# Kernel optimization log

Measured on AMD Instinct MI355X. Metric: run time of the kernel, lower is better.

## Reference

```python
import jax, jax.numpy as jnp
import numpy as np

B, S, W = 128, 128, 16          # batch, sentence len, chars per word
WV, CV = 50000, 500             # word / char vocab sizes
WE, CE, H = 128, 64, 256        # word emb, char emb (=char lstm hidden), sentence lstm hidden
NT = 25                         # tagset size
K = NT + 2                      # +START/+STOP for CRF
F = 4                           # feature_size = len(features)-1 ('CEM' consumed)
START, STOP = NT, NT + 1


def setup_inputs() -> dict:
    key = jax.random.key(0)
    ks = jax.random.split(key, 32)
    p = lambda i, shape: jax.random.normal(ks[i], shape, jnp.float32) * 0.1
    inp = {}
    inp["words2ix"] = jax.random.randint(ks[0], (B, S), 0, WV)
    inp["chars2ix"] = jax.random.randint(ks[1], (B, S, W), 0, CV)
    inp["features"] = jax.random.uniform(ks[2], (B, F, S), jnp.float32)
    lens = jax.random.randint(ks[3], (B,), S // 2, S + 1)
    inp["attention_mask"] = (jnp.arange(S)[None, :] < lens[:, None]).astype(jnp.int32)
    inp["word_emb"] = p(4, (WV, WE))
    inp["char_emb"] = p(5, (CV, CE))
    for d, i0 in (("f", 6), ("b", 10)):
        inp[f"char_Wih_{d}"] = p(i0, (4 * CE, CE))
        inp[f"char_Whh_{d}"] = p(i0 + 1, (4 * CE, CE))
        inp[f"char_bih_{d}"] = p(i0 + 2, (4 * CE,))
        inp[f"char_bhh_{d}"] = p(i0 + 3, (4 * CE,))
    inp["char_out_W"] = p(14, (CE, 2 * CE))
    inp["char_out_b"] = p(15, (CE,))
    inp["feat_W"] = p(16, (H // 2, F))
    inp["feat_b"] = p(17, (H // 2,))
    IN = WE + CE + H // 2  # 320
    for d, i0 in (("f", 18), ("b", 22)):
        inp[f"lstm_Wih_{d}"] = p(i0, (4 * H, IN))
        inp[f"lstm_Whh_{d}"] = p(i0 + 1, (4 * H, H))
        inp[f"lstm_bih_{d}"] = p(i0 + 2, (4 * H,))
        inp[f"lstm_bhh_{d}"] = p(i0 + 3, (4 * H,))
    FC = 2 * H + CE + H // 2  # 704
    inp["tag_W"] = p(26, (K, FC))
    inp["tag_b"] = p(27, (K,))
    inp["trans"] = p(28, (K, K))  # trans[i, j] = score of transition i -> j
    return inp


def _lstm(x, Wih, Whh, bih, bhh, reverse=False):
    # x: [T, N, In] -> (outputs [T, N, H], final hidden [N, H]); PyTorch gate order i,f,g,o
    Hd = Whh.shape[1]
    N = x.shape[1]

    def step(carry, xt):
        h, c = carry
        g = xt @ Wih.T + bih + h @ Whh.T + bhh
        i, f, gg, o = jnp.split(g, 4, axis=-1)
        c = jax.nn.sigmoid(f) * c + jax.nn.sigmoid(i) * jnp.tanh(gg)
        h = jax.nn.sigmoid(o) * jnp.tanh(c)
        return (h, c), h

    init = (jnp.zeros((N, Hd), x.dtype), jnp.zeros((N, Hd), x.dtype))
    (hT, _), hs = jax.lax.scan(step, init, x, reverse=reverse)
    return hs, hT


def _viterbi(feats, mask, trans):
    # feats: [B, S, K] emissions; mask: [B, S] prefix mask; trans: [K, K]
    score0 = feats[:, 0] + trans[START][None, :]  # [B, K]

    def step(score, inputs):
        feat_t, m_t = inputs                               # [B,K], [B]
        cand = score[:, :, None] + trans[None, :, :]       # [B, K_prev, K_cur]
        best = jnp.max(cand, axis=1) + feat_t              # [B, K]
        bp = jnp.argmax(cand, axis=1)                      # [B, K]
        m = (m_t > 0)[:, None]
        new_score = jnp.where(m, best, score)
        bp = jnp.where(m, bp, jnp.arange(feats.shape[-1])[None, :])
        return new_score, bp

    xs = (feats[:, 1:].transpose(1, 0, 2), mask[:, 1:].T)
    last_score, bps = jax.lax.scan(step, score0, xs)       # bps: [S-1, B, K]
    final = last_score + trans[:, STOP][None, :]
    path_score = jnp.max(final, axis=-1)                   # [B]
    last_tag = jnp.argmax(final, axis=-1)                  # [B]

    def back(tag, bp):
        prev = jnp.take_along_axis(bp, tag[:, None], axis=1)[:, 0]
        return prev, tag

    first_tag, rest = jax.lax.scan(back, last_tag, bps, reverse=True)  # rest[t] = tag_{t+1}
    path = jnp.concatenate([first_tag[None, :], rest], axis=0).transpose(1, 0)  # [B, S]
    return path_score, path


def reference(words2ix, chars2ix, features, attention_mask, word_emb, char_emb,
              char_Wih_f, char_Whh_f, char_bih_f, char_bhh_f,
              char_Wih_b, char_Whh_b, char_bih_b, char_bhh_b,
              char_out_W, char_out_b, feat_W, feat_b,
              lstm_Wih_f, lstm_Whh_f, lstm_bih_f, lstm_bhh_f,
              lstm_Wih_b, lstm_Whh_b, lstm_bib_placeholder=None, lstm_bih_b=None, lstm_bhh_b=None,
              tag_W=None, tag_b=None, trans=None):
    raise NotImplementedError


# real reference (the above stub is replaced below to keep the signature exact)
def reference(words2ix, chars2ix, features, attention_mask, word_emb, char_emb,
              char_Wih_f, char_Whh_f, char_bih_f, char_bhh_f,
              char_Wih_b, char_Whh_b, char_bih_b, char_bhh_b,
              char_out_W, char_out_b, feat_W, feat_b,
              lstm_Wih_f, lstm_Whh_f, lstm_bih_f, lstm_bhh_f,
              lstm_Wih_b, lstm_Whh_b, lstm_bih_b, lstm_bhh_b,
              tag_W, tag_b, trans):
    Bn, Sn, Wn = chars2ix.shape
    # --- CharEncode: per-word char BiLSTM, take final fwd/bwd hidden states ---
    ce = char_emb[chars2ix]                                # [B, S, W, CE]
    x = ce.reshape(Bn * Sn, Wn, CE).transpose(1, 0, 2)     # [W, B*S, CE]
    _, hf = _lstm(x, char_Wih_f, char_Whh_f, char_bih_f, char_bhh_f)
    _, hb = _lstm(x, char_Wih_b, char_Whh_b, char_bih_b, char_bhh_b, reverse=True)
    chvec = jnp.concatenate([hf, hb], axis=-1) @ char_out_W.T + char_out_b  # [B*S, CE]
    chvec = chvec.reshape(Bn, Sn, CE)
    # --- feature mapping + word embedding ---
    fv = features.transpose(0, 2, 1) @ feat_W.T + feat_b   # [B, S, H/2]
    we = word_emb[words2ix]                                # [B, S, WE]
    vec = jnp.concatenate([we, chvec, fv], axis=-1)        # [B, S, 320]
    # --- sentence BiLSTM ---
    xs = vec.transpose(1, 0, 2)                            # [S, B, 320]
    hsf, _ = _lstm(xs, lstm_Wih_f, lstm_Whh_f, lstm_bih_f, lstm_bhh_f)
    hsb, _ = _lstm(xs, lstm_Wih_b, lstm_Whh_b, lstm_bih_b, lstm_bhh_b, reverse=True)
    h = jnp.concatenate([hsf, hsb], axis=-1).transpose(1, 0, 2)  # [B, S, 2H]
    h = jnp.concatenate([h, chvec, fv], axis=-1)           # [B, S, 704]
    feats = h @ tag_W.T + tag_b                            # [B, S, K]
    # --- CRF Viterbi decode + softmax-argmax output ---
    path_score, path = _viterbi(feats, attention_mask, trans)
    tag_argmax = jnp.argmax(feats, axis=-1)                # argmax(softmax(feats)) == argmax(feats)
    return path_score, path, tag_argmax
```

## Files before the change

kernel.cpp:

```cpp
#include <hip/hip_runtime.h>
#include <stddef.h>


typedef float f32x4 __attribute__((ext_vector_type(4)));

__device__ __forceinline__ float sigm(float x){ return 1.0f/(1.0f + expf(-x)); }

__global__ __launch_bounds__(256) void k_fv(const float* __restrict__ feat,
                                            const float* __restrict__ fW,
                                            const float* __restrict__ fb,
                                            float* __restrict__ fvb)
{
  int idx = blockIdx.x*256 + threadIdx.x;
  int j = idx & 127;
  int r = idx >> 7;
  int b = r >> 7, sw = r & 127;
  const float* x = feat + b*512 + sw;
  float a = fb[j];
  a = fmaf(x[0],   fW[j*4+0], a);
  a = fmaf(x[128], fW[j*4+1], a);
  a = fmaf(x[256], fW[j*4+2], a);
  a = fmaf(x[384], fW[j*4+3], a);
  fvb[idx] = a;
}

__global__ __launch_bounds__(256) void k_gxc(
  const float* __restrict__ char_emb,
  const float* __restrict__ Wih_f, const float* __restrict__ bih_f, const float* __restrict__ bhh_f,
  const float* __restrict__ Wih_b, const float* __restrict__ bih_b, const float* __restrict__ bhh_b,
  float* __restrict__ tab)
{
  int idx = blockIdx.x*256 + threadIdx.x;
  int gi = idx & 255;
  int c  = (idx >> 8) % 500;
  int d  = idx / (500*256);
  const float* Wih = d ? Wih_b : Wih_f;
  int orig = (gi&3)*64 + (gi>>2);
  const float* w = Wih + orig*64;
  const float* e = char_emb + c*64;
  float a = (d?bih_b:bih_f)[orig] + (d?bhh_b:bhh_f)[orig];
  #pragma unroll 8
  for (int k=0;k<64;k++) a = fmaf(w[k], e[k], a);
  tab[idx] = a;
}

__global__ __launch_bounds__(256) void k_char(
  const int* __restrict__ chars2ix,
  const float* __restrict__ Whh_f, const float* __restrict__ Whh_b,
  const float* __restrict__ tab, float* __restrict__ chh)
{
  __shared__ __align__(16) float hbuf[8][64];
  __shared__ float gbuf[8][256];
  int tid = threadIdx.x, bid = blockIdx.x;
  int dir = bid >> 11, chunk = bid & 2047;
  int seq0 = chunk*8;
  const float* Whh = dir ? Whh_b : Whh_f;
  int orig = (tid&3)*64 + (tid>>2);
  float4 wr[16];
  #pragma unroll
  for (int k4=0;k4<16;k4++) wr[k4] = *(const float4*)(Whh + orig*64 + k4*4);
  for (int i=tid;i<8*64;i+=256) ((float*)hbuf)[i]=0.f;
  __syncthreads();
  const float* tb = tab + (size_t)dir*500*256;
  int u = tid & 63;
  int s0 = tid >> 6;
  float c0 = 0.f, c1 = 0.f;

  for (int t=0;t<16;t++){
    int tpos = dir ? 15-t : t;
    float acc[8];
    #pragma unroll
    for (int i=0;i<8;i++)
      acc[i] = tb[(size_t)chars2ix[(seq0+i)*16 + tpos]*256 + tid];
    #pragma unroll
    for (int k4=0;k4<16;k4++){
      float4 w = wr[k4];
      #pragma unroll
      for (int i=0;i<8;i++){
        const float4 h = *(const float4*)&hbuf[i][k4*4];
        acc[i] = fmaf(h.x,w.x, fmaf(h.y,w.y, fmaf(h.z,w.z, fmaf(h.w,w.w, acc[i]))));
      }
    }
    #pragma unroll
    for (int i=0;i<8;i++) gbuf[i][tid] = acc[i];
    __syncthreads();
    float gi0=gbuf[s0  ][u*4+0], gf0=gbuf[s0  ][u*4+1], gg0=gbuf[s0  ][u*4+2], go0=gbuf[s0  ][u*4+3];
    float gi1=gbuf[s0+4][u*4+0], gf1=gbuf[s0+4][u*4+1], gg1=gbuf[s0+4][u*4+2], go1=gbuf[s0+4][u*4+3];
    c0 = sigm(gf0)*c0 + sigm(gi0)*tanhf(gg0);
    c1 = sigm(gf1)*c1 + sigm(gi1)*tanhf(gg1);
    hbuf[s0  ][u] = sigm(go0)*tanhf(c0);
    hbuf[s0+4][u] = sigm(go1)*tanhf(c1);
    __syncthreads();
  }
  #pragma unroll
  for (int i=0;i<2;i++){
    int sq = s0 + i*4;
    chh[(size_t)(dir*16384 + seq0 + sq)*64 + u] = hbuf[sq][u];
  }
}

__global__ __launch_bounds__(256) void k_chvec(
  const float* __restrict__ chh,
  const float* __restrict__ W2, const float* __restrict__ b2,
  float* __restrict__ chvec)
{
  __shared__ __align__(16) float Wc[64*128];
  __shared__ __align__(16) float gout[4][8][64];
  int tid = threadIdx.x, bid = blockIdx.x;
  for (int i=tid;i<64*32;i+=256){
    int l2=i>>5, k4=i&31;
    *(float4*)&Wc[(l2*128 + k4*4) ^ ((l2&7)<<2)] = *(const float4*)(W2 + l2*128 + k4*4);
  }
  __syncthreads();
  int wave = __builtin_amdgcn_readfirstlane((int)(tid>>6));
  int l = tid & 63;
  float bb = b2[l];
  for (int it=0; it<2; ++it){
    int r0 = bid*64 + it*32 + wave*8;
    float acc[8];
    #pragma unroll
    for (int i=0;i<8;i++) acc[i]=bb;
    const float* hf[8]; const float* hb[8];
    #pragma unroll
    for (int i=0;i<8;i++){ hf[i]=chh+(size_t)(r0+i)*64; hb[i]=chh+(size_t)(16384+r0+i)*64; }
    #pragma unroll
    for (int k4=0;k4<16;k4++){
      float4 w=*(const float4*)&Wc[(l*128+k4*4)^((l&7)<<2)];
      #pragma unroll
      for (int i=0;i<8;i++){
        const float4 x=*(const float4*)(hf[i]+k4*4);
        acc[i]=fmaf(x.x,w.x,fmaf(x.y,w.y,fmaf(x.z,w.z,fmaf(x.w,w.w,acc[i]))));
      }
    }
    #pragma unroll
    for (int k4=0;k4<16;k4++){
      float4 w=*(const float4*)&Wc[(l*128+64+k4*4)^((l&7)<<2)];
      #pragma unroll
      for (int i=0;i<8;i++){
        const float4 x=*(const float4*)(hb[i]+k4*4);
        acc[i]=fmaf(x.x,w.x,fmaf(x.y,w.y,fmaf(x.z,w.z,fmaf(x.w,w.w,acc[i]))));
      }
    }
    #pragma unroll
    for (int i=0;i<8;i++) gout[wave][i][l]=acc[i];
    int rsub=l>>3, cg=l&7;
    #pragma unroll
    for (int i2=0;i2<2;i2++){
      int col=cg*8+i2*4;
      *(float4*)&chvec[(size_t)(r0+rsub)*64+col] = *(const float4*)&gout[wave][rsub][col];
    }
  }
}

__global__ __launch_bounds__(256, 2) void k_gxall(
  const int* __restrict__ words2ix, const float* __restrict__ word_emb,
  const float* __restrict__ chvec, const float* __restrict__ fvb,
  const float* __restrict__ Wih_f, const float* __restrict__ bih_f, const float* __restrict__ bhh_f,
  const float* __restrict__ Wih_b, const float* __restrict__ bih_b, const float* __restrict__ bhh_b,
  float* __restrict__ gxf, float* __restrict__ gxb)
{
  __shared__ __align__(16) float Wg[128*160];
  int tid=threadIdx.x, bid=blockIdx.x;
  int ct2 = bid & 7, dir = (bid>>3)&1, rch = bid>>4;
  const float* Wih = dir ? Wih_b : Wih_f;
  const float* bihp = dir ? bih_b : bih_f;
  const float* bhhp = dir ? bhh_b : bhh_f;
  float* gx = dir ? gxb : gxf;
  int wave = __builtin_amdgcn_readfirstlane((int)(tid>>6));
  int l = tid & 63;
  int swz = (l&7)<<2;
  float bias0, bias1;
  { int g0 = ct2*128 + l;      int o0 = (g0&3)*256 + (g0>>2); bias0 = bihp[o0]+bhhp[o0];
    int g1 = ct2*128 + 64 + l; int o1 = (g1&3)*256 + (g1>>2); bias1 = bihp[o1]+bhhp[o1]; }
  float acc[4][2][8];
  #pragma unroll
  for (int it=0; it<4; ++it)
    #pragma unroll
    for (int rr=0; rr<8; ++rr){ acc[it][0][rr]=bias0; acc[it][1][rr]=bias1; }

  for (int i=tid; i<128*40; i+=256){
    int g = i/40, k4 = i%40;
    int gg = ct2*128 + g, orig = (gg&3)*256 + (gg>>2);
    *(float4*)&Wg[(g*160 + k4*4) ^ ((g&7)<<2)] = *(const float4*)(Wih + orig*320 + k4*4);
  }
  __syncthreads();
  #pragma unroll
  for (int it=0; it<4; ++it){
    const float *wp[8], *cp[8];
    #pragma unroll
    for (int rr=0; rr<8; ++rr){
      int r = rch*128 + it*32 + wave*8 + rr;
      int b=r&127, sw=r>>7; int rid=b*128+sw;
      wp[rr] = word_emb + (size_t)words2ix[rid]*128;
      cp[rr] = chvec + (size_t)rid*64;
    }
    for (int k4=0;k4<32;k4++){
      float4 w0=*(const float4*)&Wg[(l*160 + k4*4) ^ swz];
      float4 w1=*(const float4*)&Wg[((l+64)*160 + k4*4) ^ swz];
      #pragma unroll
      for (int rr=0; rr<8; ++rr){
        const float4 x=*(const float4*)(wp[rr]+k4*4);
        acc[it][0][rr]=fmaf(x.x,w0.x,fmaf(x.y,w0.y,fmaf(x.z,w0.z,fmaf(x.w,w0.w,acc[it][0][rr]))));
        acc[it][1][rr]=fmaf(x.x,w1.x,fmaf(x.y,w1.y,fmaf(x.z,w1.z,fmaf(x.w,w1.w,acc[it][1][rr]))));
      }
    }
    for (int k4=32;k4<40;k4++){
      float4 w0=*(const float4*)&Wg[(l*160 + k4*4) ^ swz];
      float4 w1=*(const float4*)&Wg[((l+64)*160 + k4*4) ^ swz];
      #pragma unroll
      for (int rr=0; rr<8; ++rr){
        const float4 x=*(const float4*)(cp[rr]+(k4-32)*4);
        acc[it][0][rr]=fmaf(x.x,w0.x,fmaf(x.y,w0.y,fmaf(x.z,w0.z,fmaf(x.w,w0.w,acc[it][0][rr]))));
        acc[it][1][rr]=fmaf(x.x,w1.x,fmaf(x.y,w1.y,fmaf(x.z,w1.z,fmaf(x.w,w1.w,acc[it][1][rr]))));
      }
    }
  }
  __syncthreads();
  for (int i=tid; i<128*40; i+=256){
    int g = i/40, k4 = i%40;
    int gg = ct2*128 + g, orig = (gg&3)*256 + (gg>>2);
    *(float4*)&Wg[(g*160 + k4*4) ^ ((g&7)<<2)] = *(const float4*)(Wih + orig*320 + 160 + k4*4);
  }
  __syncthreads();
  #pragma unroll
  for (int it=0; it<4; ++it){
    const float *cp[8], *fp[8];
    #pragma unroll
    for (int rr=0; rr<8; ++rr){
      int r = rch*128 + it*32 + wave*8 + rr;
      int b=r&127, sw=r>>7; int rid=b*128+sw;
      cp[rr] = chvec + (size_t)rid*64;
      fp[rr] = fvb + (size_t)rid*128;
    }
    for (int k4=0;k4<8;k4++){
      float4 w0=*(const float4*)&Wg[(l*160 + k4*4) ^ swz];
      float4 w1=*(const float4*)&Wg[((l+64)*160 + k4*4) ^ swz];
      #pragma unroll
      for (int rr=0; rr<8; ++rr){
        const float4 x=*(const float4*)(cp[rr]+32+k4*4);
        acc[it][0][rr]=fmaf(x.x,w0.x,fmaf(x.y,w0.y,fmaf(x.z,w0.z,fmaf(x.w,w0.w,acc[it][0][rr]))));
        acc[it][1][rr]=fmaf(x.x,w1.x,fmaf(x.y,w1.y,fmaf(x.z,w1.z,fmaf(x.w,w1.w,acc[it][1][rr]))));
      }
    }
    for (int k4=8;k4<40;k4++){
      float4 w0=*(const float4*)&Wg[(l*160 + k4*4) ^ swz];
      float4 w1=*(const float4*)&Wg[((l+64)*160 + k4*4) ^ swz];
      #pragma unroll
      for (int rr=0; rr<8; ++rr){
        const float4 x=*(const float4*)(fp[rr]+(k4-8)*4);
        acc[it][0][rr]=fmaf(x.x,w0.x,fmaf(x.y,w0.y,fmaf(x.z,w0.z,fmaf(x.w,w0.w,acc[it][0][rr]))));
        acc[it][1][rr]=fmaf(x.x,w1.x,fmaf(x.y,w1.y,fmaf(x.z,w1.z,fmaf(x.w,w1.w,acc[it][1][rr]))));
      }
    }
  }
  #pragma unroll
  for (int it=0; it<4; ++it)
    #pragma unroll
    for (int rr=0; rr<8; ++rr){
      int r = rch*128 + it*32 + wave*8 + rr;
      gx[(size_t)r*1024 + ct2*128 + l]      = acc[it][0][rr];
      gx[(size_t)r*1024 + ct2*128 + 64 + l] = acc[it][1][rr];
    }
}

__global__ __launch_bounds__(512, 2) void k_sent(
  const float* __restrict__ gxf, const float* __restrict__ gxb,
  const float* __restrict__ Whh_f, const float* __restrict__ Whh_b,
  float* __restrict__ hA, float* __restrict__ hB,
  float* __restrict__ hsf, float* __restrict__ hsb,
  unsigned int* __restrict__ cnt)
{
  __shared__ __align__(16) float Wl[128*260];
  __shared__ __align__(16) float hstage[8*264];
  __shared__ float gbuf[8*16*10];
  int tid=threadIdx.x, bid=blockIdx.x;
  int gt = bid & 7, dir = (bid>>3)&1, chunk = bid>>4;
  int grp = bid >> 3;
  unsigned int* ctr = cnt + (grp<<6);
  const float* Whh = dir ? Whh_b : Whh_f;
  const float* gx  = dir ? gxb : gxf;
  float* hs = dir ? hsb : hsf;
  int b0 = chunk*8;

  for (int i=tid; i<128*64; i+=512){
    int g = i>>6, k4 = i&63;
    int gi = gt*128 + g, orig = (gi&3)*256 + (gi>>2);
    *(float4*)&Wl[g*260 + k4*4] = *(const float4*)(Whh + orig*256 + k4*4);
  }
  for (int i=tid; i<8*264; i+=512) hstage[i] = 0.f;
  __syncthreads();

  int wave = tid>>6, l = tid&63;
  int gl = l & 15, ng = l >> 4;
  int grow = wave*16 + gl;
  int ul = l >> 3, nn = l & 7;
  int au = gt*32 + wave*4 + ul;
  float creg = 0.f;
  float nxt[2];
  {
    int spos0 = dir ? 127 : 0;
    #pragma unroll
    for (int i=0;i<2;i++)
      nxt[i] = gx[(size_t)(spos0*128 + b0 + ng*2 + i)*1024 + gt*128 + grow];
  }

  for (int t=0; t<128; ++t){
    int spos = dir ? 127 - t : t;
    float acc0 = nxt[0], acc1 = nxt[1];
    if (t < 127){
      int sposn = dir ? 126 - t : t+1;
      #pragma unroll
      for (int i=0;i<2;i++)
        nxt[i] = gx[(size_t)(sposn*128 + b0 + ng*2 + i)*1024 + gt*128 + grow];
    }
    #pragma unroll 8
    for (int k4=0;k4<64;k4++){
      float4 w  = *(const float4*)&Wl[grow*260 + k4*4];
      float4 x0 = *(const float4*)&hstage[(ng*2+0)*264 + k4*4];
      float4 x1 = *(const float4*)&hstage[(ng*2+1)*264 + k4*4];
      acc0 = fmaf(x0.x,w.x, fmaf(x0.y,w.y, fmaf(x0.z,w.z, fmaf(x0.w,w.w, acc0))));
      acc1 = fmaf(x1.x,w.x, fmaf(x1.y,w.y, fmaf(x1.z,w.z, fmaf(x1.w,w.w, acc1))));
    }
    gbuf[(wave*16 + gl)*10 + ng*2+0] = acc0;
    gbuf[(wave*16 + gl)*10 + ng*2+1] = acc1;
    if (l < 32){
      float g_i = gbuf[(wave*16 + ul*4+0)*10 + nn];
      float g_f = gbuf[(wave*16 + ul*4+1)*10 + nn];
      float g_g = gbuf[(wave*16 + ul*4+2)*10 + nn];
      float g_o = gbuf[(wave*16 + ul*4+3)*10 + nn];
      creg = sigm(g_f)*creg + sigm(g_i)*tanhf(g_g);
      float h = sigm(g_o)*tanhf(creg);
      float* hn = ((t&1)==0) ? hB : hA;
      __hip_atomic_store(&hn[(size_t)(dir*128 + b0 + nn)*256 + au], h,
                         __ATOMIC_RELAXED, __HIP_MEMORY_SCOPE_AGENT);
      hs[(size_t)(spos*128 + b0 + nn)*256 + au] = h;
    }
    __syncthreads();
    if (tid==0){
      atomicAdd(ctr, 1u);
      unsigned int target = 8u*(unsigned)(t+1);
      while (__hip_atomic_load(ctr, __ATOMIC_RELAXED, __HIP_MEMORY_SCOPE_AGENT) < target)
        __builtin_amdgcn_s_sleep(2);
    }
    __syncthreads();
    if (t < 127){
      const float* hc = ((t&1)==0) ? hB : hA;
      int row = tid >> 6, col4 = (tid & 63) * 4;
      const float* p = &hc[(size_t)(dir*128 + b0 + row)*256 + col4];
      f32x4 v;
      asm volatile("global_load_dwordx4 %0, %1, off sc0 sc1"
                   : "=v"(v) : "v"(p) : "memory");
      asm volatile("s_waitcnt vmcnt(0)" ::: "memory");
      __builtin_amdgcn_sched_barrier(0);
      *(f32x4*)&hstage[row*264 + col4] = v;
      __syncthreads();
    }
  }
}

__global__ __launch_bounds__(256) void k_feats(
  const float* __restrict__ hsf, const float* __restrict__ hsb,
  const float* __restrict__ chvec, const float* __restrict__ fvb,
  const float* __restrict__ tagW, const float* __restrict__ tagb,
  float* __restrict__ feats)
{
  __shared__ __align__(16) float Wt[27*352];
  int tid=threadIdx.x, bid=blockIdx.x;
  int wave=__builtin_amdgcn_readfirstlane((int)(tid>>6));
  int l=tid&63;
  int r0=bid*32+wave*8;
  bool act = (l < 27);
  float acc[8];
  #pragma unroll
  for (int i=0;i<8;i++) acc[i] = act ? tagb[l] : 0.f;
  const float* hfr[8]; const float* hbr[8]; const float* cr[8]; const float* fr[8];
  #pragma unroll
  for (int i=0;i<8;i++){
    int r=r0+i; int b=r>>7, sw=r&127;
    hfr[i]=hsf + (size_t)(sw*128+b)*256;
    hbr[i]=hsb + (size_t)(sw*128+b)*256;
    cr[i]=chvec + (size_t)r*64;
    fr[i]=fvb + (size_t)r*128;
  }
  for (int i=tid;i<27*88;i+=256){
    int rr=i/88, k4=i%88;
    *(float4*)&Wt[(rr*352+k4*4)^((rr&7)<<2)] = *(const float4*)(tagW + rr*704 + k4*4);
  }
  __syncthreads();
  if (act){
    for (int k4=0;k4<64;k4++){
      float4 w=*(const float4*)&Wt[(l*352+k4*4)^((l&7)<<2)];
      #pragma unroll
      for (int i=0;i<8;i++){
        const float4 x=*(const float4*)(hfr[i]+k4*4);
        acc[i]=fmaf(x.x,w.x,fmaf(x.y,w.y,fmaf(x.z,w.z,fmaf(x.w,w.w,acc[i]))));
      }
    }
    for (int k4=64;k4<88;k4++){
      float4 w=*(const float4*)&Wt[(l*352+k4*4)^((l&7)<<2)];
      #pragma unroll
      for (int i=0;i<8;i++){
        const float4 x=*(const float4*)(hbr[i]+(k4-64)*4);
        acc[i]=fmaf(x.x,w.x,fmaf(x.y,w.y,fmaf(x.z,w.z,fmaf(x.w,w.w,acc[i]))));
      }
    }
  }
  __syncthreads();
  for (int i=tid;i<27*88;i+=256){
    int rr=i/88, k4=i%88;
    *(float4*)&Wt[(rr*352+k4*4)^((rr&7)<<2)] = *(const float4*)(tagW + rr*704 + 352 + k4*4);
  }
  __syncthreads();
  if (act){
    for (int k4=0;k4<40;k4++){
      float4 w=*(const float4*)&Wt[(l*352+k4*4)^((l&7)<<2)];
      #pragma unroll
      for (int i=0;i<8;i++){
        const float4 x=*(const float4*)(hbr[i]+96+k4*4);
        acc[i]=fmaf(x.x,w.x,fmaf(x.y,w.y,fmaf(x.z,w.z,fmaf(x.w,w.w,acc[i]))));
      }
    }
    for (int k4=40;k4<56;k4++){
      float4 w=*(const float4*)&Wt[(l*352+k4*4)^((l&7)<<2)];
      #pragma unroll
      for (int i=0;i<8;i++){
        const float4 x=*(const float4*)(cr[i]+(k4-40)*4);
        acc[i]=fmaf(x.x,w.x,fmaf(x.y,w.y,fmaf(x.z,w.z,fmaf(x.w,w.w,acc[i]))));
      }
    }
    for (int k4=56;k4<88;k4++){
      float4 w=*(const float4*)&Wt[(l*352+k4*4)^((l&7)<<2)];
      #pragma unroll
      for (int i=0;i<8;i++){
        const float4 x=*(const float4*)(fr[i]+(k4-56)*4);
        acc[i]=fmaf(x.x,w.x,fmaf(x.y,w.y,fmaf(x.z,w.z,fmaf(x.w,w.w,acc[i]))));
      }
    }
    #pragma unroll
    for (int i=0;i<8;i++) feats[(size_t)(r0+i)*27 + l] = acc[i];
  }
}

__global__ __launch_bounds__(256) void k_argmax(const float* __restrict__ feats,
                                                float* __restrict__ out)
{
  int r = blockIdx.x*256 + threadIdx.x;
  const float* f = feats + (size_t)r*27;
  float best = f[0]; int bi = 0;
  #pragma unroll
  for (int j=1;j<27;j++){ float v=f[j]; if (v>best){best=v;bi=j;} }
  out[r] = (float)bi;
}

__global__ __launch_bounds__(64) void k_viterbi(
  const float* __restrict__ feats, const int* __restrict__ mask,
  const float* __restrict__ trans, float* __restrict__ out)
{
  __shared__ float tr[729];
  __shared__ unsigned char bp[127][27];
  __shared__ int tags[128];
  int b = blockIdx.x, l = threadIdx.x;
  for (int i=l;i<729;i+=64) tr[i]=trans[i];
  __syncthreads();
  int ll = (l<27) ? l : 0;
  float trc[27];
  #pragma unroll
  for (int i=0;i<27;i++) trc[i]=tr[i*27+ll];
  const float* fb_ = feats + (size_t)b*128*27;
  float score = fb_[ll] + tr[25*27 + ll];
  for (int t=1;t<128;t++){
    float best=-3.0e38f; int bi=0;
    #pragma unroll 1
    for (int i=0;i<27;i++){
      float si = __shfl(score, i, 64);
      float cand = si + trc[i];
      if (cand > best){ best=cand; bi=i; }
    }
    int m = mask[b*128 + t];
    float ns = best + fb_[t*27 + ll];
    if (m) score = ns;
    int bpv = m ? bi : ll;
    if (l < 27) bp[t-1][l] = (unsigned char)bpv;
  }
  float fin = score + tr[ll*27 + 26];
  if (l >= 27) fin = -3.0e38f;
  float bestf=-3.0e38f; int bt=0;
  #pragma unroll 1
  for (int i=0;i<27;i++){
    float v=__shfl(fin, i, 64);
    if (v > bestf){ bestf=v; bt=i; }
  }
  if (l==0){
    out[b]=bestf;
    int tg=bt; tags[127]=tg;
    for (int t=126;t>=0;t--){ tg = bp[t][tg]; tags[t]=tg; }
  }
  __syncthreads();
  float* op = out + 128 + b*128;
  for (int t=l;t<128;t+=64) op[t]=(float)tags[t];
}

extern "C" void kernel_launch(void* const* d_in, const int* in_sizes, int n_in,
                              void* d_out, int out_size, void* d_ws, size_t ws_size,
                              hipStream_t stream)
{
  (void)in_sizes; (void)n_in; (void)out_size; (void)ws_size;
  const int*   words2ix = (const int*)d_in[0];
  const int*   chars2ix = (const int*)d_in[1];
  const float* features = (const float*)d_in[2];
  const int*   amask    = (const int*)d_in[3];
  const float* word_emb = (const float*)d_in[4];
  const float* char_emb = (const float*)d_in[5];
  const float* cWih_f=(const float*)d_in[6],  *cWhh_f=(const float*)d_in[7];
  const float* cbih_f=(const float*)d_in[8],  *cbhh_f=(const float*)d_in[9];
  const float* cWih_b=(const float*)d_in[10], *cWhh_b=(const float*)d_in[11];
  const float* cbih_b=(const float*)d_in[12], *cbhh_b=(const float*)d_in[13];
  const float* coW=(const float*)d_in[14], *cob=(const float*)d_in[15];
  const float* fW =(const float*)d_in[16], *fb =(const float*)d_in[17];
  const float* lWih_f=(const float*)d_in[18], *lWhh_f=(const float*)d_in[19];
  const float* lbih_f=(const float*)d_in[20], *lbhh_f=(const float*)d_in[21];
  const float* lWih_b=(const float*)d_in[22], *lWhh_b=(const float*)d_in[23];
  const float* lbih_b=(const float*)d_in[24], *lbhh_b=(const float*)d_in[25];
  const float* tagW=(const float*)d_in[26], *tagb=(const float*)d_in[27];
  const float* trans=(const float*)d_in[28];
  float* out = (float*)d_out;

  float* p = (float*)d_ws;
  float* chvec = p; p += 16384*64;
  float* fvb   = p; p += 16384*128;
  float* gxf   = p; p += (size_t)16384*1024;
  float* gxb   = p; p += (size_t)16384*1024;
  float* chh   = p; p += 2*16384*64;
  float* tab   = p; p += 2*500*256;
  float* hA    = p; p += 2*128*256;
  float* hB    = p; p += 2*128*256;
  float* hsf   = p; p += (size_t)128*128*256;
  float* hsb   = p; p += (size_t)128*128*256;
  float* feats = p; p += 16384*27;
  unsigned int* cnt = (unsigned int*)p;

  hipMemsetAsync(cnt, 0, 32*64*sizeof(unsigned int), stream);

  k_gxc<<<1000,256,0,stream>>>(char_emb, cWih_f,cbih_f,cbhh_f, cWih_b,cbih_b,cbhh_b, tab);
  k_fv<<<8192,256,0,stream>>>(features, fW, fb, fvb);
  k_char<<<4096,256,0,stream>>>(chars2ix, cWhh_f, cWhh_b, tab, chh);
  k_chvec<<<256,256,0,stream>>>(chh, coW, cob, chvec);
  k_gxall<<<2048,256,0,stream>>>(words2ix, word_emb, chvec, fvb,
      lWih_f,lbih_f,lbhh_f, lWih_b,lbih_b,lbhh_b, gxf, gxb);
  k_sent<<<256,512,0,stream>>>(gxf, gxb, lWhh_f, lWhh_b, hA, hB, hsf, hsb, cnt);
  k_feats<<<512,256,0,stream>>>(hsf, hsb, chvec, fvb, tagW, tagb, feats);
  k_argmax<<<64,256,0,stream>>>(feats, out + 128 + 16384);
  k_viterbi<<<128,64,0,stream>>>(feats, amask, trans, out);
}
```

Baseline: 2.567 ms.

## Halve gate tile in input-projection GEMM, transpose weights in LDS, double grid

The input-projection kernel now gives each block 64 gate columns instead of 128. Its weight tile is stored transposed in shared memory so each lane reads scalar weights instead of swizzled float4 rows. The accumulator count per thread halves, launch bounds rise to 4 blocks per CU and the grid doubles to 4096 blocks, all aimed at higher occupancy. In exchange each block reuses its activation loads (word embedding, chvec, fvb) across half as many output columns, so global and cache traffic for activations roughly doubles.

```diff
diff --git a/kernel.cpp b/kernel.cpp
--- a/kernel.cpp
+++ b/kernel.cpp
@@ -152,114 +152,121 @@
   }
 }
 
-__global__ __launch_bounds__(256, 2) void k_gxall(
+__global__ __launch_bounds__(256, 4) void k_gxall(
   const int* __restrict__ words2ix, const float* __restrict__ word_emb,
   const float* __restrict__ chvec, const float* __restrict__ fvb,
   const float* __restrict__ Wih_f, const float* __restrict__ bih_f, const float* __restrict__ bhh_f,
   const float* __restrict__ Wih_b, const float* __restrict__ bih_b, const float* __restrict__ bhh_b,
   float* __restrict__ gxf, float* __restrict__ gxb)
 {
-  __shared__ __align__(16) float Wg[128*160];
+  __shared__ float Wt[160*64];
   int tid=threadIdx.x, bid=blockIdx.x;
-  int ct2 = bid & 7, dir = (bid>>3)&1, rch = bid>>4;
+  int ct = bid & 15, dir = (bid>>4)&1, rch = bid>>5;
   const float* Wih = dir ? Wih_b : Wih_f;
   const float* bihp = dir ? bih_b : bih_f;
   const float* bhhp = dir ? bhh_b : bhh_f;
   float* gx = dir ? gxb : gxf;
   int wave = __builtin_amdgcn_readfirstlane((int)(tid>>6));
   int l = tid & 63;
-  int swz = (l&7)<<2;
-  float bias0, bias1;
-  { int g0 = ct2*128 + l;      int o0 = (g0&3)*256 + (g0>>2); bias0 = bihp[o0]+bhhp[o0];
-    int g1 = ct2*128 + 64 + l; int o1 = (g1&3)*256 + (g1>>2); bias1 = bihp[o1]+bhhp[o1]; }
-  float acc[4][2][8];
+  float acc[4][8];
+  {
+    int gg = ct*64 + l, og = (gg&3)*256 + (gg>>2);
+    float bias = bihp[og] + bhhp[og];
+    #pragma unroll
+    for (int it=0; it<4; ++it)
+      #pragma unroll
+      for (int rr=0; rr<8; ++rr) acc[it][rr] = bias;
+  }
+
+  for (int i=tid; i<64*40; i+=256){
+    int g = i & 63, q = i >> 6;
+    int gg = ct*64 + g, orig = (gg&3)*256 + (gg>>2);
+    float4 v = *(const float4*)(Wih + orig*320 + q*4);
+    Wt[(q*4+0)*64 + g] = v.x;
+    Wt[(q*4+1)*64 + g] = v.y;
+    Wt[(q*4+2)*64 + g] = v.z;
+    Wt[(q*4+3)*64 + g] = v.w;
+  }
+  __syncthreads();
+  #pragma unroll
+  for (int it=0; it<4; ++it){
+    int ob = it*32 + wave*8;
+    const float* xr[8];
+    #pragma unroll
+    for (int rr=0; rr<8; ++rr)
+      xr[rr] = word_emb + (size_t)words2ix[(ob+rr)*128 + rch]*128;
+    #pragma unroll 4
+    for (int q=0; q<32; ++q){
+      float w0=Wt[(q*4+0)*64+l], w1=Wt[(q*4+1)*64+l];
+      float w2=Wt[(q*4+2)*64+l], w3=Wt[(q*4+3)*64+l];
+      #pragma unroll
+      for (int rr=0; rr<8; ++rr){
+        const float4 x = *(const float4*)(xr[rr] + q*4);
+        acc[it][rr] = fmaf(x.x,w0, fmaf(x.y,w1, fmaf(x.z,w2, fmaf(x.w,w3, acc[it][rr]))));
+      }
+    }
+    #pragma unroll
+    for (int rr=0; rr<8; ++rr)
+      xr[rr] = chvec + (size_t)((ob+rr)*128 + rch)*64;
+    #pragma unroll
+    for (int q=32; q<40; ++q){
+      float w0=Wt[(q*4+0)*64+l], w1=Wt[(q*4+1)*64+l];
+      float w2=Wt[(q*4+2)*64+l], w3=Wt[(q*4+3)*64+l];
+      #pragma unroll
+      for (int rr=0; rr<8; ++rr){
+        const float4 x = *(const float4*)(xr[rr] + (q-32)*4);
+        acc[it][rr] = fmaf(x.x,w0, fmaf(x.y,w1, fmaf(x.z,w2, fmaf(x.w,w3, acc[it][rr]))));
+      }
+    }
+  }
+  __syncthreads();
+  for (int i=tid; i<64*40; i+=256){
+    int g = i & 63, q = i >> 6;
+    int gg = ct*64 + g, orig = (gg&3)*256 + (gg>>2);
+    float4 v = *(const float4*)(Wih + orig*320 + 160 + q*4);
+    Wt[(q*4+0)*64 + g] = v.x;
+    Wt[(q*4+1)*64 + g] = v.y;
+    Wt[(q*4+2)*64 + g] = v.z;
+    Wt[(q*4+3)*64 + g] = v.w;
+  }
+  __syncthreads();
+  #pragma unroll
+  for (int it=0; it<4; ++it){
+    int ob = it*32 + wave*8;
+    const float* xr[8];
+    #pragma unroll
+    for (int rr=0; rr<8; ++rr)
+      xr[rr] = chvec + (size_t)((ob+rr)*128 + rch)*64;
+    #pragma unroll
+    for (int q=0; q<8; ++q){
+      float w0=Wt[(q*4+0)*64+l], w1=Wt[(q*4+1)*64+l];
+      float w2=Wt[(q*4+2)*64+l], w3=Wt[(q*4+3)*64+l];
+      #pragma unroll
+      for (int rr=0; rr<8; ++rr){
+        const float4 x = *(const float4*)(xr[rr] + 32 + q*4);
+        acc[it][rr] = fmaf(x.x,w0, fmaf(x.y,w1, fmaf(x.z,w2, fmaf(x.w,w3, acc[it][rr]))));
+      }
+    }
+    #pragma unroll
+    for (int rr=0; rr<8; ++rr)
+      xr[rr] = fvb + (size_t)((ob+rr)*128 + rch)*128;
+    #pragma unroll 4
+    for (int q=8; q<40; ++q){
+      float w0=Wt[(q*4+0)*64+l], w1=Wt[(q*4+1)*64+l];
+      float w2=Wt[(q*4+2)*64+l], w3=Wt[(q*4+3)*64+l];
+      #pragma unroll
+      for (int rr=0; rr<8; ++rr){
+        const float4 x = *(const float4*)(xr[rr] + (q-8)*4);
+        acc[it][rr] = fmaf(x.x,w0, fmaf(x.y,w1, fmaf(x.z,w2, fmaf(x.w,w3, acc[it][rr]))));
+      }
+    }
+  }
   #pragma unroll
   for (int it=0; it<4; ++it)
-    #pragma unroll
-    for (int rr=0; rr<8; ++rr){ acc[it][0][rr]=bias0; acc[it][1][rr]=bias1; }
-
-  for (int i=tid; i<128*40; i+=256){
-    int g = i/40, k4 = i%40;
-    int gg = ct2*128 + g, orig = (gg&3)*256 + (gg>>2);
-    *(float4*)&Wg[(g*160 + k4*4) ^ ((g&7)<<2)] = *(const float4*)(Wih + orig*320 + k4*4);
-  }
-  __syncthreads();
-  #pragma unroll
-  for (int it=0; it<4; ++it){
-    const float *wp[8], *cp[8];
     #pragma unroll
     for (int rr=0; rr<8; ++rr){
       int r = rch*128 + it*32 + wave*8 + rr;
-      int b=r&127, sw=r>>7; int rid=b*128+sw;
-      wp[rr] = word_emb + (size_t)words2ix[rid]*128;
-      cp[rr] = chvec + (size_t)rid*64;
-    }
-    for (int k4=0;k4<32;k4++){
-      float4 w0=*(const float4*)&Wg[(l*160 + k4*4) ^ swz];
-      float4 w1=*(const float4*)&Wg[((l+64)*160 + k4*4) ^ swz];
-      #pragma unroll
-      for (int rr=0; rr<8; ++rr){
-        const float4 x=*(const float4*)(wp[rr]+k4*4);
-        acc[it][0][rr]=fmaf(x.x,w0.x,fmaf(x.y,w0.y,fmaf(x.z,w0.z,fmaf(x.w,w0.w,acc[it][0][rr]))));
-        acc[it][1][rr]=fmaf(x.x,w1.x,fmaf(x.y,w1.y,fmaf(x.z,w1.z,fmaf(x.w,w1.w,acc[it][1][rr]))));
-      }
-    }
-    for (int k4=32;k4<40;k4++){
-      float4 w0=*(const float4*)&Wg[(l*160 + k4*4) ^ swz];
-      float4 w1=*(const float4*)&Wg[((l+64)*160 + k4*4) ^ swz];
-      #pragma unroll
-      for (int rr=0; rr<8; ++rr){
-        const float4 x=*(const float4*)(cp[rr]+(k4-32)*4);
-        acc[it][0][rr]=fmaf(x.x,w0.x,fmaf(x.y,w0.y,fmaf(x.z,w0.z,fmaf(x.w,w0.w,acc[it][0][rr]))));
-        acc[it][1][rr]=fmaf(x.x,w1.x,fmaf(x.y,w1.y,fmaf(x.z,w1.z,fmaf(x.w,w1.w,acc[it][1][rr]))));
-      }
-    }
-  }
-  __syncthreads();
-  for (int i=tid; i<128*40; i+=256){
-    int g = i/40, k4 = i%40;
-    int gg = ct2*128 + g, orig = (gg&3)*256 + (gg>>2);
-    *(float4*)&Wg[(g*160 + k4*4) ^ ((g&7)<<2)] = *(const float4*)(Wih + orig*320 + 160 + k4*4);
-  }
-  __syncthreads();
-  #pragma unroll
-  for (int it=0; it<4; ++it){
-    const float *cp[8], *fp[8];
-    #pragma unroll
-    for (int rr=0; rr<8; ++rr){
-      int r = rch*128 + it*32 + wave*8 + rr;
-      int b=r&127, sw=r>>7; int rid=b*128+sw;
-      cp[rr] = chvec + (size_t)rid*64;
-      fp[rr] = fvb + (size_t)rid*128;
-    }
-    for (int k4=0;k4<8;k4++){
-      float4 w0=*(const float4*)&Wg[(l*160 + k4*4) ^ swz];
-      float4 w1=*(const float4*)&Wg[((l+64)*160 + k4*4) ^ swz];
-      #pragma unroll
-      for (int rr=0; rr<8; ++rr){
-        const float4 x=*(const float4*)(cp[rr]+32+k4*4);
-        acc[it][0][rr]=fmaf(x.x,w0.x,fmaf(x.y,w0.y,fmaf(x.z,w0.z,fmaf(x.w,w0.w,acc[it][0][rr]))));
-        acc[it][1][rr]=fmaf(x.x,w1.x,fmaf(x.y,w1.y,fmaf(x.z,w1.z,fmaf(x.w,w1.w,acc[it][1][rr]))));
-      }
-    }
-    for (int k4=8;k4<40;k4++){
-      float4 w0=*(const float4*)&Wg[(l*160 + k4*4) ^ swz];
-      float4 w1=*(const float4*)&Wg[((l+64)*160 + k4*4) ^ swz];
-      #pragma unroll
-      for (int rr=0; rr<8; ++rr){
-        const float4 x=*(const float4*)(fp[rr]+(k4-8)*4);
-        acc[it][0][rr]=fmaf(x.x,w0.x,fmaf(x.y,w0.y,fmaf(x.z,w0.z,fmaf(x.w,w0.w,acc[it][0][rr]))));
-        acc[it][1][rr]=fmaf(x.x,w1.x,fmaf(x.y,w1.y,fmaf(x.z,w1.z,fmaf(x.w,w1.w,acc[it][1][rr]))));
-      }
-    }
-  }
-  #pragma unroll
-  for (int it=0; it<4; ++it)
-    #pragma unroll
-    for (int rr=0; rr<8; ++rr){
-      int r = rch*128 + it*32 + wave*8 + rr;
-      gx[(size_t)r*1024 + ct2*128 + l]      = acc[it][0][rr];
-      gx[(size_t)r*1024 + ct2*128 + 64 + l] = acc[it][1][rr];
+      gx[(size_t)r*1024 + ct*64 + l] = acc[it][rr];
     }
 }
 
@@ -545,7 +552,7 @@
   k_fv<<<8192,256,0,stream>>>(features, fW, fb, fvb);
   k_char<<<4096,256,0,stream>>>(chars2ix, cWhh_f, cWhh_b, tab, chh);
   k_chvec<<<256,256,0,stream>>>(chh, coW, cob, chvec);
-  k_gxall<<<2048,256,0,stream>>>(words2ix, word_emb, chvec, fvb,
+  k_gxall<<<4096,256,0,stream>>>(words2ix, word_emb, chvec, fvb,
       lWih_f,lbih_f,lbhh_f, lWih_b,lbih_b,lbhh_b, gxf, gxb);
   k_sent<<<256,512,0,stream>>>(gxf, gxb, lWhh_f, lWhh_b, hA, hB, hsf, hsb, cnt);
   k_feats<<<512,256,0,stream>>>(hsf, hsb, chvec, fvb, tagW, tagb, feats);
```

Result: faster. 2.485 ms (-3.2%).
